# Optimization experiments

Measured on AMD Instinct MI355X. Metric: run time of the kernel, lower is better.

## Reference

```python
import jax, jax.numpy as jnp
import numpy as np

NEG_INF = -1e9

def _monotonic_energy(decoder_h, key, mask, W, b, v_weight, v_g, v_bias, r):
    # decoder_h: [B, D], key: [B, L, A], W: [A, D]
    q = decoder_h @ W.T                              # [B, A]
    t = jnp.tanh(q[:, None, :] + key + b)            # [B, L, A]
    # weight-normalized v: weight = g * v / ||v|| (norm over the whole row, dim=0 weight_norm)
    v_dir = v_weight[0] / jnp.sqrt(jnp.sum(v_weight[0] ** 2))
    energy = jnp.einsum('bla,a->bl', t, v_g[0] * v_dir) + v_bias[0] + r[0]  # [B, L]
    return jnp.where(mask > 0, energy, NEG_INF)


def _linear_recurrence(a, b):
    # x_j = a_j * x_{j-1} + b_j along axis 1, x_{-1} = 0, via parallel associative scan
    def combine(c1, c2):
        a1, b1 = c1
        a2, b2 = c2
        return (a1 * a2, a2 * b1 + b2)
    _, x = jax.lax.associative_scan(combine, (a, b), axis=1)
    return x


def setup_inputs() -> dict:
    key0 = jax.random.key(0)
    ks = jax.random.split(key0, 10)
    B, L, D, A = 64, 1024, 512, 512
    decoder_h = jax.random.normal(ks[0], (B, D), dtype=jnp.float32)
    key = jax.random.normal(ks[1], (B, L, A), dtype=jnp.float32)
    encoder_outputs = jax.random.normal(ks[2], (B, L, D), dtype=jnp.float32)
    prev_att = jax.random.uniform(ks[3], (B, L), dtype=jnp.float32)
    prev_att = prev_att / jnp.sum(prev_att, axis=1, keepdims=True)  # valid attention dist
    noise = jax.random.normal(ks[4], (B, L), dtype=jnp.float32)
    mask = jnp.ones((B, L), dtype=jnp.float32)  # 1 = valid frame
    W = jax.random.normal(ks[5], (A, D), dtype=jnp.float32) * (1.0 / np.sqrt(D))
    b = jax.random.normal(ks[6], (A,), dtype=jnp.float32)
    v_weight = jax.random.normal(ks[7], (1, A), dtype=jnp.float32)
    v_g = jnp.full((1,), 1.0 / np.sqrt(A), dtype=jnp.float32)
    v_bias = jnp.zeros((1,), dtype=jnp.float32)
    r = jnp.full((1,), -1.0, dtype=jnp.float32)
    return {"decoder_h": decoder_h, "key": key, "encoder_outputs": encoder_outputs,
            "prev_att": prev_att, "noise": noise, "mask": mask,
            "W": W, "b": b, "v_weight": v_weight, "v_g": v_g, "v_bias": v_bias, "r": r}


def reference(decoder_h, key, encoder_outputs, prev_att, noise, mask, W, b, v_weight, v_g, v_bias, r):
    # MonotonicAttention.soft_recursive with prev_att given (training steps > 0)
    # end_mask marks the last valid frame of each sequence
    end_mask = mask * jnp.pad(1.0 - mask, ((0, 0), (0, 1)), constant_values=1.0)[:, 1:]
    energy = _monotonic_energy(decoder_h, key, mask, W, b, v_weight, v_g, v_bias, r)
    p_select = jax.nn.sigmoid(energy + noise)            # [B, L]
    p_select = jnp.where(end_mask > 0, end_mask, p_select)
    # shifted (1 - p_choose_{j-1}) with leading 1
    shifted = jnp.pad(1.0 - p_select[:, :-1], ((0, 0), (1, 0)), constant_values=1.0)
    # alpha_div_p_j = shifted_j * alpha_div_p_{j-1} + prev_att_j  (linear recurrence)
    alpha_div_p = _linear_recurrence(shifted, prev_att)
    alpha = p_select * alpha_div_p
    return alpha
```

## Files before the change

### kernel.cpp

```cpp
#include <hip/hip_runtime.h>
#include <math.h>

#define Bb 64
#define Ll 1024
#define Dd 512
#define Aa 512
#define NEG_INF -1e9f

#define LOG2E  1.4426950408889634f
#define LOG2E2 2.8853901617526703f
#define NCH 8

typedef float fx4 __attribute__((ext_vector_type(4)));

__device__ __forceinline__ float fast_exp2(float x) { return __builtin_amdgcn_exp2f(x); }
__device__ __forceinline__ float fast_rcp(float x)  { return __builtin_amdgcn_rcpf(x); }

__global__ __launch_bounds__(256) void k_epart(const float* __restrict__ key,
                                               const float* __restrict__ dh,
                                               const float* __restrict__ W,
                                               const float* __restrict__ bias,
                                               const float* __restrict__ vw,
                                               const float* __restrict__ vg,
                                               float* __restrict__ pw) {
    const int c     = blockIdx.x;
    const int halfl = blockIdx.y;
    const int b     = blockIdx.z;
    const int tid   = threadIdx.x;
    const int wave  = tid >> 6, lane = tid & 63;

    __shared__ float h[Dd];
    __shared__ float qs[64];
    __shared__ float vs[64];
    __shared__ float red[4];

    ((float2*)h)[tid] = ((const float2*)(dh + (size_t)b * Dd))[tid];

    {
        float w0 = vw[tid], w1 = vw[tid + 256];
        float s = fmaf(w0, w0, w1 * w1);
        #pragma unroll
        for (int off = 32; off; off >>= 1) s += __shfl_xor(s, off);
        if (lane == 0) red[wave] = s;
    }
    __syncthreads();
    const float inv = rsqrtf(red[0] + red[1] + red[2] + red[3]);
    const float g2 = 2.f * vg[0];

    {
        const int r = tid >> 2, quart = tid & 3;
        const int arow = c * 64 + r;
        const float4* Wr = (const float4*)(W + (size_t)arow * Dd + quart * 128);
        const float4* h4 = (const float4*)(h + quart * 128);
        float acc = 0.f;
        #pragma unroll 8
        for (int i = 0; i < 32; ++i) {
            float4 wq = Wr[i];
            float4 hv = h4[i];
            acc = fmaf(wq.x, hv.x, acc);
            acc = fmaf(wq.y, hv.y, acc);
            acc = fmaf(wq.z, hv.z, acc);
            acc = fmaf(wq.w, hv.w, acc);
        }
        acc += __shfl_xor(acc, 1);
        acc += __shfl_xor(acc, 2);
        if (quart == 0) {
            qs[r] = (acc + bias[arow]) * LOG2E2;
            vs[r] = g2 * vw[arow] * inv;
        }
    }
    __syncthreads();

    const int sub = lane & 7;
    fx4 q0 = *(const fx4*)&qs[sub * 4];
    fx4 q1 = *(const fx4*)&qs[32 + sub * 4];
    fx4 v0 = *(const fx4*)&vs[sub * 4];
    fx4 v1 = *(const fx4*)&vs[32 + sub * 4];

    const int lbase = halfl * 512 + wave * 8 + (lane >> 3);
    const float* rowp = key + ((size_t)b * Ll + lbase) * Aa + c * 64;
    float* pwp = pw + (((size_t)b * Ll + lbase) * NCH) + c;

    #pragma unroll 4
    for (int it = 0; it < 16; ++it) {
        const float* rp = rowp + (size_t)it * 32 * Aa;
        fx4 ka = *(const fx4*)(rp + sub * 4);
        fx4 kb = *(const fx4*)(rp + 32 + sub * 4);

        float acc = 0.f;
        acc = fmaf(v0.x, fast_rcp(fast_exp2(fmaf(ka.x, LOG2E2, q0.x)) + 1.f), acc);
        acc = fmaf(v0.y, fast_rcp(fast_exp2(fmaf(ka.y, LOG2E2, q0.y)) + 1.f), acc);
        acc = fmaf(v0.z, fast_rcp(fast_exp2(fmaf(ka.z, LOG2E2, q0.z)) + 1.f), acc);
        acc = fmaf(v0.w, fast_rcp(fast_exp2(fmaf(ka.w, LOG2E2, q0.w)) + 1.f), acc);
        acc = fmaf(v1.x, fast_rcp(fast_exp2(fmaf(kb.x, LOG2E2, q1.x)) + 1.f), acc);
        acc = fmaf(v1.y, fast_rcp(fast_exp2(fmaf(kb.y, LOG2E2, q1.y)) + 1.f), acc);
        acc = fmaf(v1.z, fast_rcp(fast_exp2(fmaf(kb.z, LOG2E2, q1.z)) + 1.f), acc);
        acc = fmaf(v1.w, fast_rcp(fast_exp2(fmaf(kb.w, LOG2E2, q1.w)) + 1.f), acc);

        acc += __shfl_xor(acc, 1);
        acc += __shfl_xor(acc, 2);
        acc += __shfl_xor(acc, 4);
        if (sub == 0) pwp[(size_t)it * 32 * NCH] = acc;
    }
}

__global__ __launch_bounds__(256) void k_finish(const float* __restrict__ pw,
                                                const float* __restrict__ noise,
                                                const float* __restrict__ mask,
                                                const float* __restrict__ prev,
                                                const float* __restrict__ vw,
                                                const float* __restrict__ vg,
                                                const float* __restrict__ vb,
                                                const float* __restrict__ r,
                                                float* __restrict__ alpha) {
    const int b = blockIdx.x;
    const int tid = threadIdx.x;
    const int wave = tid >> 6, lane = tid & 63;
    __shared__ float red[4], red2[4], pend[4], wA[4], wB[4];

    {
        float w0 = vw[tid], w1 = vw[tid + 256];
        float s = fmaf(w0, w0, w1 * w1);
        float t = w0 + w1;
        #pragma unroll
        for (int off = 32; off; off >>= 1) {
            s += __shfl_xor(s, off);
            t += __shfl_xor(t, off);
        }
        if (lane == 0) { red[wave] = s; red2[wave] = t; }
    }
    __syncthreads();
    const float inv = rsqrtf(red[0] + red[1] + red[2] + red[3]);
    const float sumv = red2[0] + red2[1] + red2[2] + red2[3];
    const float ec = vg[0] * inv * sumv + vb[0] + r[0];

    const int l0 = tid * 4;
    const float* pwb = pw + ((size_t)b * Ll + l0) * NCH;
    fx4 s0a = *(const fx4*)(pwb + 0),  s0b = *(const fx4*)(pwb + 4);
    fx4 s1a = *(const fx4*)(pwb + 8),  s1b = *(const fx4*)(pwb + 12);
    fx4 s2a = *(const fx4*)(pwb + 16), s2b = *(const fx4*)(pwb + 20);
    fx4 s3a = *(const fx4*)(pwb + 24), s3b = *(const fx4*)(pwb + 28);
    float e0 = ((s0a.x + s0a.y) + (s0a.z + s0a.w)) + ((s0b.x + s0b.y) + (s0b.z + s0b.w));
    float e1 = ((s1a.x + s1a.y) + (s1a.z + s1a.w)) + ((s1b.x + s1b.y) + (s1b.z + s1b.w));
    float e2 = ((s2a.x + s2a.y) + (s2a.z + s2a.w)) + ((s2b.x + s2b.y) + (s2b.z + s2b.w));
    float e3 = ((s3a.x + s3a.y) + (s3a.z + s3a.w)) + ((s3b.x + s3b.y) + (s3b.z + s3b.w));

    const float4 nz = ((const float4*)(noise + (size_t)b * Ll))[tid];
    const float4 mk = ((const float4*)(mask + (size_t)b * Ll))[tid];
    const float mk4 = (tid == 255) ? 0.f : mask[(size_t)b * Ll + l0 + 4];

    float4 pp;
    {
        float e, z, pv, em;
        e = (mk.x > 0.f) ? (ec - e0) : NEG_INF; z = e + nz.x;
        pv = fast_rcp(1.f + fast_exp2(-z * LOG2E));
        em = mk.x * (1.f - mk.y); pp.x = (em > 0.f) ? em : pv;
        e = (mk.y > 0.f) ? (ec - e1) : NEG_INF; z = e + nz.y;
        pv = fast_rcp(1.f + fast_exp2(-z * LOG2E));
        em = mk.y * (1.f - mk.z); pp.y = (em > 0.f) ? em : pv;
        e = (mk.z > 0.f) ? (ec - e2) : NEG_INF; z = e + nz.z;
        pv = fast_rcp(1.f + fast_exp2(-z * LOG2E));
        em = mk.z * (1.f - mk.w); pp.z = (em > 0.f) ? em : pv;
        e = (mk.w > 0.f) ? (ec - e3) : NEG_INF; z = e + nz.w;
        pv = fast_rcp(1.f + fast_exp2(-z * LOG2E));
        em = mk.w * (1.f - mk4); pp.w = (em > 0.f) ? em : pv;
    }

    if (lane == 63) pend[wave] = pp.w;
    __syncthreads();
    float pm1 = __shfl_up(pp.w, 1);
    if (lane == 0) pm1 = (wave == 0) ? 0.f : pend[wave - 1];

    const float4 pa = ((const float4*)(prev + (size_t)b * Ll))[tid];
    const float a0 = 1.f - pm1;
    const float a1 = 1.f - pp.x;
    const float a2 = 1.f - pp.y;
    const float a3 = 1.f - pp.z;

    float A = a0, Bv = pa.x;
    Bv = fmaf(a1, Bv, pa.y); A *= a1;
    Bv = fmaf(a2, Bv, pa.z); A *= a2;
    Bv = fmaf(a3, Bv, pa.w); A *= a3;

    float Ai = A, Bi = Bv;
    #pragma unroll
    for (int off = 1; off < 64; off <<= 1) {
        float qA = __shfl_up(Ai, off);
        float qB = __shfl_up(Bi, off);
        if (lane >= off) { Bi = fmaf(Ai, qB, Bi); Ai *= qA; }
    }
    float eA = __shfl_up(Ai, 1), eB = __shfl_up(Bi, 1);
    if (lane == 0) { eA = 1.f; eB = 0.f; }
    if (lane == 63) { wA[wave] = Ai; wB[wave] = Bi; }
    __syncthreads();
    float bwe = 0.f;
    for (int w2 = 0; w2 < wave; ++w2) bwe = fmaf(wA[w2], bwe, wB[w2]);
    float x = fmaf(eA, bwe, eB);

    float4 o;
    x = fmaf(a0, x, pa.x); o.x = pp.x * x;
    x = fmaf(a1, x, pa.y); o.y = pp.y * x;
    x = fmaf(a2, x, pa.z); o.z = pp.z * x;
    x = fmaf(a3, x, pa.w); o.w = pp.w * x;
    ((float4*)(alpha + (size_t)b * Ll))[tid] = o;
}

extern "C" void kernel_launch(void* const* d_in, const int* in_sizes, int n_in,
                              void* d_out, int out_size, void* d_ws, size_t ws_size,
                              hipStream_t stream) {
    const float* dh    = (const float*)d_in[0];
    const float* key   = (const float*)d_in[1];
    const float* prev  = (const float*)d_in[3];
    const float* noise = (const float*)d_in[4];
    const float* mask  = (const float*)d_in[5];
    const float* W     = (const float*)d_in[6];
    const float* bias  = (const float*)d_in[7];
    const float* vw    = (const float*)d_in[8];
    const float* vg    = (const float*)d_in[9];
    const float* vb    = (const float*)d_in[10];
    const float* r     = (const float*)d_in[11];
    float* out = (float*)d_out;

    float* pw = (float*)d_ws;

    k_epart<<<dim3(NCH, 2, Bb), 256, 0, stream>>>(key, dh, W, bias, vw, vg, pw);
    k_finish<<<Bb, 256, 0, stream>>>(pw, noise, mask, prev, vw, vg, vb, r, out);
}
```

Baseline: 48.02 us.

## Batch 16 key-row loads per thread and stage partial energies in shared memory

The energy kernel now uses one block per (A-chunk, batch), so the grid shrinks from 1024 to 512 blocks. Each 16-lane group covers a 64-wide A chunk and issues 16 independent row loads before any compute, which raises memory-level parallelism. Partials are stored in shared memory and written to the workspace in a chunk-major layout, so the finish kernel sums them with contiguous vector loads. The cost is higher register pressure, fewer blocks (each doing twice the work and computing the W·h projection once instead of twice), and a wider 16-lane shuffle reduction.

```diff
diff --git a/kernel.cpp b/kernel.cpp
--- a/kernel.cpp
+++ b/kernel.cpp
@@ -9,12 +9,23 @@
 
 #define LOG2E  1.4426950408889634f
 #define LOG2E2 2.8853901617526703f
-#define NCH 8
 
 typedef float fx4 __attribute__((ext_vector_type(4)));
 
 __device__ __forceinline__ float fast_exp2(float x) { return __builtin_amdgcn_exp2f(x); }
 __device__ __forceinline__ float fast_rcp(float x)  { return __builtin_amdgcn_rcpf(x); }
+
+#define TERM4(ACC, K, Q, V)                                                   \
+    ACC = fmaf(V.x, fast_rcp(fast_exp2(fmaf(K.x, LOG2E2, Q.x)) + 1.f), ACC);  \
+    ACC = fmaf(V.y, fast_rcp(fast_exp2(fmaf(K.y, LOG2E2, Q.y)) + 1.f), ACC);  \
+    ACC = fmaf(V.z, fast_rcp(fast_exp2(fmaf(K.z, LOG2E2, Q.z)) + 1.f), ACC);  \
+    ACC = fmaf(V.w, fast_rcp(fast_exp2(fmaf(K.w, LOG2E2, Q.w)) + 1.f), ACC);
+
+#define RED16(A)                   \
+    A += __shfl_xor(A, 1);         \
+    A += __shfl_xor(A, 2);         \
+    A += __shfl_xor(A, 4);         \
+    A += __shfl_xor(A, 8);
 
 __global__ __launch_bounds__(256) void k_epart(const float* __restrict__ key,
                                                const float* __restrict__ dh,
@@ -23,16 +34,17 @@
                                                const float* __restrict__ vw,
                                                const float* __restrict__ vg,
                                                float* __restrict__ pw) {
-    const int c     = blockIdx.x;
-    const int halfl = blockIdx.y;
-    const int b     = blockIdx.z;
-    const int tid   = threadIdx.x;
-    const int wave  = tid >> 6, lane = tid & 63;
+    const int c = blockIdx.x;
+    const int b = blockIdx.y;
+    const int tid = threadIdx.x;
+    const int wave = tid >> 6, lane = tid & 63;
+    const int g = lane >> 4, sub = lane & 15;
 
     __shared__ float h[Dd];
     __shared__ float qs[64];
     __shared__ float vs[64];
     __shared__ float red[4];
+    __shared__ float pl[Ll];
 
     ((float2*)h)[tid] = ((const float2*)(dh + (size_t)b * Dd))[tid];
 
@@ -45,7 +57,7 @@
     }
     __syncthreads();
     const float inv = rsqrtf(red[0] + red[1] + red[2] + red[3]);
-    const float g2 = 2.f * vg[0];
+    const float g2i = 2.f * vg[0] * inv;
 
     {
         const int r = tid >> 2, quart = tid & 3;
@@ -66,42 +78,69 @@
         acc += __shfl_xor(acc, 2);
         if (quart == 0) {
             qs[r] = (acc + bias[arow]) * LOG2E2;
-            vs[r] = g2 * vw[arow] * inv;
-        }
-    }
-    __syncthreads();
-
-    const int sub = lane & 7;
-    fx4 q0 = *(const fx4*)&qs[sub * 4];
-    fx4 q1 = *(const fx4*)&qs[32 + sub * 4];
-    fx4 v0 = *(const fx4*)&vs[sub * 4];
-    fx4 v1 = *(const fx4*)&vs[32 + sub * 4];
-
-    const int lbase = halfl * 512 + wave * 8 + (lane >> 3);
-    const float* rowp = key + ((size_t)b * Ll + lbase) * Aa + c * 64;
-    float* pwp = pw + (((size_t)b * Ll + lbase) * NCH) + c;
-
-    #pragma unroll 4
-    for (int it = 0; it < 16; ++it) {
-        const float* rp = rowp + (size_t)it * 32 * Aa;
-        fx4 ka = *(const fx4*)(rp + sub * 4);
-        fx4 kb = *(const fx4*)(rp + 32 + sub * 4);
-
-        float acc = 0.f;
-        acc = fmaf(v0.x, fast_rcp(fast_exp2(fmaf(ka.x, LOG2E2, q0.x)) + 1.f), acc);
-        acc = fmaf(v0.y, fast_rcp(fast_exp2(fmaf(ka.y, LOG2E2, q0.y)) + 1.f), acc);
-        acc = fmaf(v0.z, fast_rcp(fast_exp2(fmaf(ka.z, LOG2E2, q0.z)) + 1.f), acc);
-        acc = fmaf(v0.w, fast_rcp(fast_exp2(fmaf(ka.w, LOG2E2, q0.w)) + 1.f), acc);
-        acc = fmaf(v1.x, fast_rcp(fast_exp2(fmaf(kb.x, LOG2E2, q1.x)) + 1.f), acc);
-        acc = fmaf(v1.y, fast_rcp(fast_exp2(fmaf(kb.y, LOG2E2, q1.y)) + 1.f), acc);
-        acc = fmaf(v1.z, fast_rcp(fast_exp2(fmaf(kb.z, LOG2E2, q1.z)) + 1.f), acc);
-        acc = fmaf(v1.w, fast_rcp(fast_exp2(fmaf(kb.w, LOG2E2, q1.w)) + 1.f), acc);
-
-        acc += __shfl_xor(acc, 1);
-        acc += __shfl_xor(acc, 2);
-        acc += __shfl_xor(acc, 4);
-        if (sub == 0) pwp[(size_t)it * 32 * NCH] = acc;
-    }
+            vs[r] = g2i * vw[arow];
+        }
+    }
+    __syncthreads();
+
+    const fx4 q0 = ((const fx4*)qs)[sub];
+    const fx4 v0 = ((const fx4*)vs)[sub];
+    const float* kbase = key + ((size_t)b * Ll) * Aa + c * 64 + sub * 4;
+
+    #pragma unroll 1
+    for (int it = 0; it < 4; ++it) {
+        const int base = it * 256 + wave * 64 + g * 16;
+        const float* kp = kbase + (size_t)base * Aa;
+        fx4 k0 = *(const fx4*)(kp + 0 * Aa);
+        fx4 k1 = *(const fx4*)(kp + 1 * Aa);
+        fx4 k2 = *(const fx4*)(kp + 2 * Aa);
+        fx4 k3 = *(const fx4*)(kp + 3 * Aa);
+        fx4 k4 = *(const fx4*)(kp + 4 * Aa);
+        fx4 k5 = *(const fx4*)(kp + 5 * Aa);
+        fx4 k6 = *(const fx4*)(kp + 6 * Aa);
+        fx4 k7 = *(const fx4*)(kp + 7 * Aa);
+        fx4 k8 = *(const fx4*)(kp + 8 * Aa);
+        fx4 k9 = *(const fx4*)(kp + 9 * Aa);
+        fx4 kA = *(const fx4*)(kp + 10 * Aa);
+        fx4 kB = *(const fx4*)(kp + 11 * Aa);
+        fx4 kC = *(const fx4*)(kp + 12 * Aa);
+        fx4 kD = *(const fx4*)(kp + 13 * Aa);
+        fx4 kE = *(const fx4*)(kp + 14 * Aa);
+        fx4 kF = *(const fx4*)(kp + 15 * Aa);
+        __builtin_amdgcn_sched_barrier(0);
+
+        float a0 = 0.f, a1 = 0.f, a2 = 0.f, a3 = 0.f,
+              a4 = 0.f, a5 = 0.f, a6 = 0.f, a7 = 0.f,
+              a8 = 0.f, a9 = 0.f, aA = 0.f, aB = 0.f,
+              aC = 0.f, aD = 0.f, aE = 0.f, aF = 0.f;
+        TERM4(a0, k0, q0, v0) TERM4(a1, k1, q0, v0)
+        TERM4(a2, k2, q0, v0) TERM4(a3, k3, q0, v0)
+        TERM4(a4, k4, q0, v0) TERM4(a5, k5, q0, v0)
+        TERM4(a6, k6, q0, v0) TERM4(a7, k7, q0, v0)
+        TERM4(a8, k8, q0, v0) TERM4(a9, k9, q0, v0)
+        TERM4(aA, kA, q0, v0) TERM4(aB, kB, q0, v0)
+        TERM4(aC, kC, q0, v0) TERM4(aD, kD, q0, v0)
+        TERM4(aE, kE, q0, v0) TERM4(aF, kF, q0, v0)
+
+        RED16(a0) RED16(a1) RED16(a2) RED16(a3)
+        RED16(a4) RED16(a5) RED16(a6) RED16(a7)
+        RED16(a8) RED16(a9) RED16(aA) RED16(aB)
+        RED16(aC) RED16(aD) RED16(aE) RED16(aF)
+
+        if (sub == 0) {
+            pl[base + 0]  = a0; pl[base + 1]  = a1;
+            pl[base + 2]  = a2; pl[base + 3]  = a3;
+            pl[base + 4]  = a4; pl[base + 5]  = a5;
+            pl[base + 6]  = a6; pl[base + 7]  = a7;
+            pl[base + 8]  = a8; pl[base + 9]  = a9;
+            pl[base + 10] = aA; pl[base + 11] = aB;
+            pl[base + 12] = aC; pl[base + 13] = aD;
+            pl[base + 14] = aE; pl[base + 15] = aF;
+        }
+        __builtin_amdgcn_sched_barrier(0);
+    }
+    __syncthreads();
+    ((fx4*)(pw + ((size_t)b * 8 + c) * Ll))[tid] = ((const fx4*)pl)[tid];
 }
 
 __global__ __launch_bounds__(256) void k_finish(const float* __restrict__ pw,
@@ -135,15 +174,15 @@
     const float ec = vg[0] * inv * sumv + vb[0] + r[0];
 
     const int l0 = tid * 4;
-    const float* pwb = pw + ((size_t)b * Ll + l0) * NCH;
-    fx4 s0a = *(const fx4*)(pwb + 0),  s0b = *(const fx4*)(pwb + 4);
-    fx4 s1a = *(const fx4*)(pwb + 8),  s1b = *(const fx4*)(pwb + 12);
-    fx4 s2a = *(const fx4*)(pwb + 16), s2b = *(const fx4*)(pwb + 20);
-    fx4 s3a = *(const fx4*)(pwb + 24), s3b = *(const fx4*)(pwb + 28);
-    float e0 = ((s0a.x + s0a.y) + (s0a.z + s0a.w)) + ((s0b.x + s0b.y) + (s0b.z + s0b.w));
-    float e1 = ((s1a.x + s1a.y) + (s1a.z + s1a.w)) + ((s1b.x + s1b.y) + (s1b.z + s1b.w));
-    float e2 = ((s2a.x + s2a.y) + (s2a.z + s2a.w)) + ((s2b.x + s2b.y) + (s2b.z + s2b.w));
-    float e3 = ((s3a.x + s3a.y) + (s3a.z + s3a.w)) + ((s3b.x + s3b.y) + (s3b.z + s3b.w));
+    const float* pwb = pw + (size_t)b * 8 * Ll + l0;
+    fx4 es = *(const fx4*)(pwb);
+    es += *(const fx4*)(pwb + 1 * Ll);
+    es += *(const fx4*)(pwb + 2 * Ll);
+    es += *(const fx4*)(pwb + 3 * Ll);
+    es += *(const fx4*)(pwb + 4 * Ll);
+    es += *(const fx4*)(pwb + 5 * Ll);
+    es += *(const fx4*)(pwb + 6 * Ll);
+    es += *(const fx4*)(pwb + 7 * Ll);
 
     const float4 nz = ((const float4*)(noise + (size_t)b * Ll))[tid];
     const float4 mk = ((const float4*)(mask + (size_t)b * Ll))[tid];
@@ -152,16 +191,16 @@
     float4 pp;
     {
         float e, z, pv, em;
-        e = (mk.x > 0.f) ? (ec - e0) : NEG_INF; z = e + nz.x;
+        e = (mk.x > 0.f) ? (ec - es.x) : NEG_INF; z = e + nz.x;
         pv = fast_rcp(1.f + fast_exp2(-z * LOG2E));
         em = mk.x * (1.f - mk.y); pp.x = (em > 0.f) ? em : pv;
-        e = (mk.y > 0.f) ? (ec - e1) : NEG_INF; z = e + nz.y;
+        e = (mk.y > 0.f) ? (ec - es.y) : NEG_INF; z = e + nz.y;
         pv = fast_rcp(1.f + fast_exp2(-z * LOG2E));
         em = mk.y * (1.f - mk.z); pp.y = (em > 0.f) ? em : pv;
-        e = (mk.z > 0.f) ? (ec - e2) : NEG_INF; z = e + nz.z;
+        e = (mk.z > 0.f) ? (ec - es.z) : NEG_INF; z = e + nz.z;
         pv = fast_rcp(1.f + fast_exp2(-z * LOG2E));
         em = mk.z * (1.f - mk.w); pp.z = (em > 0.f) ? em : pv;
-        e = (mk.w > 0.f) ? (ec - e3) : NEG_INF; z = e + nz.w;
+        e = (mk.w > 0.f) ? (ec - es.w) : NEG_INF; z = e + nz.w;
         pv = fast_rcp(1.f + fast_exp2(-z * LOG2E));
         em = mk.w * (1.f - mk4); pp.w = (em > 0.f) ? em : pv;
     }
@@ -223,6 +262,6 @@
 
     float* pw = (float*)d_ws;
 
-    k_epart<<<dim3(NCH, 2, Bb), 256, 0, stream>>>(key, dh, W, bias, vw, vg, pw);
+    k_epart<<<dim3(8, Bb), 256, 0, stream>>>(key, dh, W, bias, vw, vg, pw);
     k_finish<<<Bb, 256, 0, stream>>>(pw, noise, mask, prev, vw, vg, vb, r, out);
 }
```

After: 39.77 us. 1.21x faster.
